# Optimization experiments

Hardware: AMD Instinct MI355X
Metric: run time of the kernel (lower is better)

Reference implementation:

```python
import jax, jax.numpy as jnp
import numpy as np
from jax import lax

B, S, D_IN, D_STATE, D_OUT, N_HEADS = 4, 2048, 2048, 2048, 2048, 16
H = D_STATE // N_HEADS  # 128


def setup_inputs() -> dict:
    key = jax.random.key(0)
    k1, k2, k3, k4, k5 = jax.random.split(key, 5)
    x = jax.random.normal(k1, (B, S, D_IN), dtype=jnp.float32)
    Wi = jax.random.normal(k2, (D_IN, D_STATE), dtype=jnp.float32) * (D_IN ** -0.5)
    b = jax.random.normal(k3, (D_STATE,), dtype=jnp.float32) * 0.01
    # state_weight is init'd with normal_ in torch; scale down for numerical sanity
    state_w = jax.random.normal(k4, (N_HEADS, H, H), dtype=jnp.float32) * (H ** -0.5)
    Wo = jax.random.normal(k5, (D_STATE, D_OUT), dtype=jnp.float32) * (D_STATE ** -0.5)
    input_state = jnp.zeros((B, D_STATE), dtype=jnp.float32)
    return {"x": x, "input_state": input_state, "Wi": Wi, "b": b,
            "state_w": state_w, "Wo": Wo}


def _rnn_forward(x, input_state, Wi, b, state_w, Wo):
    # input projection: [B,S,D_IN] -> [B,S,N,H]
    xp = (jnp.einsum('bsd,de->bse', x, Wi) + b).reshape(B, S, N_HEADS, H)
    h0 = input_state.reshape(B, N_HEADS, H)

    def step(h, xt):  # h: [B,N,H], xt: [B,N,H]
        h = jnp.tanh(jnp.einsum('bnh,nhk->bnk', h, state_w) + xt)
        return h, h

    _, hs = lax.scan(step, h0, jnp.moveaxis(xp, 1, 0))  # hs: [S,B,N,H]
    hs = jnp.moveaxis(hs, 0, 1)                         # [B,S,N,H]
    output_state = hs[:, -1].reshape(B, D_STATE)        # [B, state_size]
    out = jnp.einsum('bsd,de->bse', hs.reshape(B, S, D_STATE), Wo)
    return out, output_state


def reference(x, input_state, Wi, b, state_w, Wo):
    return _rnn_forward(x, input_state, Wi, b, state_w, Wo)
```

## Files before the change

kernel.cpp:

```cpp
#include <hip/hip_runtime.h>
#include <hip/hip_bf16.h>

#define B_ 4
#define S_ 2048
#define DIN 2048
#define DST 2048
#define DOUT 2048
#define NH 16
#define HH 128
#define M_ (B_ * S_)
#define OUT_OFF ((size_t)M_ * DOUT)

typedef __attribute__((ext_vector_type(8))) __bf16 bf16x8;
typedef __attribute__((ext_vector_type(4))) float f32x4;
typedef __attribute__((ext_vector_type(2))) _Float16 f16x2;

__device__ __forceinline__ unsigned short f2bf(float f) {
    unsigned int u = __float_as_uint(f);
    unsigned int r = u + 0x7FFFu + ((u >> 16) & 1u);
    return (unsigned short)(r >> 16);
}
__device__ __forceinline__ unsigned pk16(_Float16 a, _Float16 b) {
    return (unsigned)__builtin_bit_cast(unsigned short, a) |
           ((unsigned)__builtin_bit_cast(unsigned short, b) << 16);
}

__device__ __forceinline__ float fdot2(f16x2 a, f16x2 b, float c) {
#if __has_builtin(__builtin_amdgcn_fdot2)
    return __builtin_amdgcn_fdot2(a, b, c, false);
#else
    return fmaf((float)a.x, (float)b.x, fmaf((float)a.y, (float)b.y, c));
#endif
}
__device__ __forceinline__ float fdu(unsigned h, unsigned w, float c) {
    return fdot2(__builtin_bit_cast(f16x2, h), __builtin_bit_cast(f16x2, w), c);
}

__device__ __forceinline__ void gload_lds16(const void* g, void* l) {
    __builtin_amdgcn_global_load_lds(
        (const __attribute__((address_space(1))) void*)g,
        (__attribute__((address_space(3))) void*)l, 16, 0, 0);
}

__global__ __launch_bounds__(256) void k_transpose_bf16(
    const float* __restrict__ in, unsigned short* __restrict__ out, int K, int N) {
    __shared__ float tile[64][65];
    int k0 = blockIdx.y * 64, n0 = blockIdx.x * 64;
    int tr  = threadIdx.x >> 4;
    int tc4 = (threadIdx.x & 15) * 4;
#pragma unroll
    for (int p = 0; p < 4; ++p) {
        int r = tr + p * 16;
        float4 v = *(const float4*)&in[(size_t)(k0 + r) * N + n0 + tc4];
        tile[r][tc4 + 0] = v.x; tile[r][tc4 + 1] = v.y;
        tile[r][tc4 + 2] = v.z; tile[r][tc4 + 3] = v.w;
    }
    __syncthreads();
#pragma unroll
    for (int p = 0; p < 4; ++p) {
        int n = tr + p * 16;
        ushort4 o;
        o.x = f2bf(tile[tc4 + 0][n]); o.y = f2bf(tile[tc4 + 1][n]);
        o.z = f2bf(tile[tc4 + 2][n]); o.w = f2bf(tile[tc4 + 3][n]);
        *(ushort4*)&out[(size_t)(n0 + n) * K + k0 + tc4] = o;
    }
}

__global__ __launch_bounds__(256, 2) void k_gemm1(
    const float* __restrict__ x,
    const unsigned short* __restrict__ Bt,
    unsigned short* __restrict__ xpf,
    const float* __restrict__ bias) {
    __shared__ unsigned short As[128 * 64];
    __shared__ unsigned short Bs[128 * 64];
    const int tid  = threadIdx.x;
    const int lane = tid & 63;
    const int wid  = tid >> 6;
    const int wr = wid >> 1, wc = wid & 1;
    const int row0 = blockIdx.y * 128, col0 = blockIdx.x * 128;

    f32x4 acc[4][4];
#pragma unroll
    for (int m = 0; m < 4; ++m)
#pragma unroll
        for (int n = 0; n < 4; ++n) acc[m][n] = (f32x4)(0.f);

    const float* Ab = x + (size_t)row0 * DIN;
    const char* Bb = (const char*)(Bt + (size_t)col0 * DIN);

    int srow[4], skb[4];
#pragma unroll
    for (int i = 0; i < 4; ++i) {
        unsigned o = (unsigned)(i * 256 + tid) * 16u;
        unsigned l = o ^ (((o >> 7) & 7u) << 4);
        srow[i] = (int)(l >> 7);
        skb[i]  = (int)(l & 127u);
    }

    for (int kt = 0; kt < DIN; kt += 64) {
#pragma unroll
        for (int i = 0; i < 8; ++i) {
            int idx = i * 256 + tid;
            int row = idx >> 4;
            int cc  = (idx & 15) * 4;
            float4 v = *(const float4*)&Ab[(size_t)row * DIN + kt + cc];
            ushort4 u;
            u.x = f2bf(v.x); u.y = f2bf(v.y); u.z = f2bf(v.z); u.w = f2bf(v.w);
            unsigned byte = (unsigned)(row * 128 + cc * 2);
            byte ^= ((unsigned)(row & 7)) << 4;
            *(ushort4*)((char*)As + byte) = u;
        }
#pragma unroll
        for (int i = 0; i < 4; ++i) {
            unsigned o = (unsigned)(i * 256 + tid) * 16u;
            gload_lds16(Bb + (size_t)srow[i] * (DIN * 2) + (size_t)kt * 2 + skb[i],
                        (char*)Bs + o);
        }
        asm volatile("s_waitcnt vmcnt(0)" ::: "memory");
        __syncthreads();
#pragma unroll
        for (int ks = 0; ks < 2; ++ks) {
            bf16x8 af[4], bfr[4];
#pragma unroll
            for (int m = 0; m < 4; ++m) {
                int row = wr * 64 + m * 16 + (lane & 15);
                unsigned o = (unsigned)(row * 128 + ks * 64 + ((lane >> 4) * 16));
                o ^= ((unsigned)(row & 7) << 4);
                af[m] = *(const bf16x8*)((const char*)As + o);
            }
#pragma unroll
            for (int n = 0; n < 4; ++n) {
                int col = wc * 64 + n * 16 + (lane & 15);
                unsigned o = (unsigned)(col * 128 + ks * 64 + ((lane >> 4) * 16));
                o ^= ((unsigned)(col & 7) << 4);
                bfr[n] = *(const bf16x8*)((const char*)Bs + o);
            }
#pragma unroll
            for (int m = 0; m < 4; ++m)
#pragma unroll
                for (int n = 0; n < 4; ++n)
                    acc[m][n] = __builtin_amdgcn_mfma_f32_16x16x32_bf16(
                        af[m], bfr[n], acc[m][n], 0, 0, 0);
        }
        __syncthreads();
    }

#pragma unroll
    for (int n = 0; n < 4; ++n) {
        int gcol = col0 + wc * 64 + n * 16 + (lane & 15);
        float bv = bias[gcol];
#pragma unroll
        for (int m = 0; m < 4; ++m) {
            int growb = row0 + wr * 64 + m * 16 + ((lane >> 4) * 4);
#pragma unroll
            for (int r = 0; r < 4; ++r) {
                float v = acc[m][n][r] + bv;
                xpf[(size_t)(growb + r) * DST + gcol] =
                    __builtin_bit_cast(unsigned short, (_Float16)v);
            }
        }
    }
}

__global__ __launch_bounds__(256, 2) void k_gemm2(
    const unsigned short* __restrict__ A,
    const unsigned short* __restrict__ Bt,
    float* __restrict__ C) {
    __shared__ unsigned short As[128 * 64];
    __shared__ unsigned short Bs[128 * 64];
    const int tid  = threadIdx.x;
    const int lane = tid & 63;
    const int wid  = tid >> 6;
    const int wr = wid >> 1, wc = wid & 1;
    const int row0 = blockIdx.y * 128, col0 = blockIdx.x * 128;

    f32x4 acc[4][4];
#pragma unroll
    for (int m = 0; m < 4; ++m)
#pragma unroll
        for (int n = 0; n < 4; ++n) acc[m][n] = (f32x4)(0.f);

    const char* Abase = (const char*)(A + (size_t)row0 * DST);
    const char* Bbase = (const char*)(Bt + (size_t)col0 * DST);

    int srow[4], skb[4];
#pragma unroll
    for (int i = 0; i < 4; ++i) {
        unsigned o = (unsigned)(i * 256 + tid) * 16u;
        unsigned l = o ^ (((o >> 7) & 7u) << 4);
        srow[i] = (int)(l >> 7);
        skb[i]  = (int)(l & 127u);
    }

    for (int kt = 0; kt < DST; kt += 64) {
#pragma unroll
        for (int i = 0; i < 4; ++i) {
            unsigned o = (unsigned)(i * 256 + tid) * 16u;
            gload_lds16(Abase + (size_t)srow[i] * (DST * 2) + (size_t)kt * 2 + skb[i],
                        (char*)As + o);
            gload_lds16(Bbase + (size_t)srow[i] * (DST * 2) + (size_t)kt * 2 + skb[i],
                        (char*)Bs + o);
        }
        asm volatile("s_waitcnt vmcnt(0)" ::: "memory");
        __syncthreads();
#pragma unroll
        for (int ks = 0; ks < 2; ++ks) {
            bf16x8 af[4], bfr[4];
#pragma unroll
            for (int m = 0; m < 4; ++m) {
                int row = wr * 64 + m * 16 + (lane & 15);
                unsigned o = (unsigned)(row * 128 + ks * 64 + ((lane >> 4) * 16));
                o ^= ((unsigned)(row & 7) << 4);
                af[m] = *(const bf16x8*)((const char*)As + o);
            }
#pragma unroll
            for (int n = 0; n < 4; ++n) {
                int col = wc * 64 + n * 16 + (lane & 15);
                unsigned o = (unsigned)(col * 128 + ks * 64 + ((lane >> 4) * 16));
                o ^= ((unsigned)(col & 7) << 4);
                bfr[n] = *(const bf16x8*)((const char*)Bs + o);
            }
#pragma unroll
            for (int m = 0; m < 4; ++m)
#pragma unroll
                for (int n = 0; n < 4; ++n)
                    acc[m][n] = __builtin_amdgcn_mfma_f32_16x16x32_bf16(
                        af[m], bfr[n], acc[m][n], 0, 0, 0);
        }
        __syncthreads();
    }

#pragma unroll
    for (int n = 0; n < 4; ++n) {
        int gcol = col0 + wc * 64 + n * 16 + (lane & 15);
#pragma unroll
        for (int m = 0; m < 4; ++m) {
            int growb = row0 + wr * 64 + m * 16 + ((lane >> 4) * 4);
            float* cp = C + (size_t)growb * DOUT + gcol;
#pragma unroll
            for (int r = 0; r < 4; ++r) cp[(size_t)r * DOUT] = acc[m][n][r];
        }
    }
}

__global__ __attribute__((amdgpu_flat_work_group_size(64, 64),
                          amdgpu_waves_per_eu(1, 1))) void k_scan(
    const unsigned short* __restrict__ xpf,
    const float* __restrict__ h0,
    const float* __restrict__ sw,
    unsigned short* __restrict__ hsb,
    float* __restrict__ out_state) {
    __shared__ __align__(16) unsigned hb[64];
    const int l = threadIdx.x;
    const int bb = blockIdx.x >> 4;
    const int nn = blockIdx.x & 15;
    const int c0 = l * 2;

    const float* wb = sw + (size_t)nn * HH * HH;

    unsigned wu[128];
#pragma unroll
    for (int k = 0; k < 64; ++k) {
        float2 rA = *(const float2*)&wb[(size_t)(2 * k) * HH + c0];
        float2 rB = *(const float2*)&wb[(size_t)(2 * k + 1) * HH + c0];
        unsigned a = pk16((_Float16)rA.x, (_Float16)rB.x);
        unsigned b = pk16((_Float16)rA.y, (_Float16)rB.y);
        asm volatile("" : "+v"(a));
        asm volatile("" : "+v"(b));
        wu[k] = a;
        wu[64 + k] = b;
    }

    {
        float2 h2 = *(const float2*)&h0[bb * DST + nn * HH + c0];
        hb[l] = pk16((_Float16)h2.x, (_Float16)h2.y);
    }

    const unsigned* xrow = (const unsigned*)(xpf + (size_t)bb * S_ * DST + nn * HH) + l;
    unsigned* hrow = (unsigned*)(hsb + (size_t)bb * S_ * DST + nn * HH) + l;
    float* osp = out_state + bb * DST + nn * HH + c0;

    unsigned x0 = xrow[0], x1 = xrow[1024], x2 = xrow[2048], x3 = xrow[3072];

    const uint4* hp = (const uint4*)hb;

    for (int t = 0; t < S_; ++t) {
        int tpf = (t + 4 < S_) ? t + 4 : S_ - 1;
        unsigned x4 = xrow[(size_t)tpf * 1024];

        float a0 = 0.f, a1 = 0.f, a2 = 0.f, a3 = 0.f;
        float b0 = 0.f, b1 = 0.f, b2 = 0.f, b3 = 0.f;
#pragma unroll
        for (int j = 0; j < 16; ++j) {
            uint4 H = hp[j];
            a0 = fdu(H.x, wu[4 * j + 0], a0); b0 = fdu(H.x, wu[64 + 4 * j + 0], b0);
            a1 = fdu(H.y, wu[4 * j + 1], a1); b1 = fdu(H.y, wu[64 + 4 * j + 1], b1);
            a2 = fdu(H.z, wu[4 * j + 2], a2); b2 = fdu(H.z, wu[64 + 4 * j + 2], b2);
            a3 = fdu(H.w, wu[4 * j + 3], a3); b3 = fdu(H.w, wu[64 + 4 * j + 3], b3);
        }

        f16x2 xv = __builtin_bit_cast(f16x2, x0);
        float s0 = ((a0 + a1) + (a2 + a3)) + (float)xv.x;
        float s1 = ((b0 + b1) + (b2 + b3)) + (float)xv.y;
        float e0 = __builtin_amdgcn_exp2f(s0 * 2.885390081777927f);
        float e1 = __builtin_amdgcn_exp2f(s1 * 2.885390081777927f);
        float th0 = fmaf(-2.f, __builtin_amdgcn_rcpf(e0 + 1.f), 1.f);
        float th1 = fmaf(-2.f, __builtin_amdgcn_rcpf(e1 + 1.f), 1.f);

        hb[l] = pk16((_Float16)th0, (_Float16)th1);
        hrow[(size_t)t * (DST / 2)] = (unsigned)f2bf(th0) | ((unsigned)f2bf(th1) << 16);
        if (t == S_ - 1) { osp[0] = th0; osp[1] = th1; }

        x0 = x1; x1 = x2; x2 = x3; x3 = x4;
    }
}

extern "C" void kernel_launch(void* const* d_in, const int* in_sizes, int n_in,
                              void* d_out, int out_size, void* d_ws, size_t ws_size,
                              hipStream_t stream) {
    const float* x    = (const float*)d_in[0];
    const float* h0   = (const float*)d_in[1];
    const float* Wi   = (const float*)d_in[2];
    const float* bias = (const float*)d_in[3];
    const float* sw   = (const float*)d_in[4];
    const float* Wo   = (const float*)d_in[5];
    float* out = (float*)d_out;

    char* ws = (char*)d_ws;
    unsigned short* hsb = (unsigned short*)ws;
    unsigned short* wit = (unsigned short*)(ws + 33554432);
    unsigned short* wot = (unsigned short*)(ws + 41943040);
    unsigned short* xpf = (unsigned short*)(ws + 50331648);

    dim3 tg(32, 32);
    k_transpose_bf16<<<tg, 256, 0, stream>>>(Wi, wit, DIN, DST);
    k_transpose_bf16<<<tg, 256, 0, stream>>>(Wo, wot, DST, DOUT);
    dim3 g1(DST / 128, M_ / 128);
    k_gemm1<<<g1, 256, 0, stream>>>(x, wit, xpf, bias);
    k_scan<<<64, 64, 0, stream>>>(xpf, h0, sw, hsb, out + OUT_OFF);
    dim3 g2(DOUT / 128, M_ / 128);
    k_gemm2<<<g2, 256, 0, stream>>>(hsb, wot, out);
}
```

Baseline: 1.043 ms.

## Rewrite recurrent scan with MFMA per head, batching all batch rows

Replaces the per-(batch, head) single-wave scan, which used fdot2 with weights held in registers, with one 256-thread block per head. Each step computes the recurrent matvec for all 4 batch rows at once using 16x16x32 f16 MFMA, padding the batch dimension to 16. The hidden state is double-buffered in swizzled LDS with one barrier per step. This cuts the ALU dot-product work on the serial critical path, at the cost of a block barrier each step, 12 of 16 MFMA columns wasted on padding, and only 16 blocks running.

```diff
diff --git a/kernel.cpp b/kernel.cpp
--- a/kernel.cpp
+++ b/kernel.cpp
@@ -14,6 +14,7 @@
 typedef __attribute__((ext_vector_type(8))) __bf16 bf16x8;
 typedef __attribute__((ext_vector_type(4))) float f32x4;
 typedef __attribute__((ext_vector_type(2))) _Float16 f16x2;
+typedef __attribute__((ext_vector_type(8))) _Float16 f16x8;
 
 __device__ __forceinline__ unsigned short f2bf(float f) {
     unsigned int u = __float_as_uint(f);
@@ -23,17 +24,6 @@
 __device__ __forceinline__ unsigned pk16(_Float16 a, _Float16 b) {
     return (unsigned)__builtin_bit_cast(unsigned short, a) |
            ((unsigned)__builtin_bit_cast(unsigned short, b) << 16);
-}
-
-__device__ __forceinline__ float fdot2(f16x2 a, f16x2 b, float c) {
-#if __has_builtin(__builtin_amdgcn_fdot2)
-    return __builtin_amdgcn_fdot2(a, b, c, false);
-#else
-    return fmaf((float)a.x, (float)b.x, fmaf((float)a.y, (float)b.y, c));
-#endif
-}
-__device__ __forceinline__ float fdu(unsigned h, unsigned w, float c) {
-    return fdot2(__builtin_bit_cast(f16x2, h), __builtin_bit_cast(f16x2, w), c);
 }
 
 __device__ __forceinline__ void gload_lds16(const void* g, void* l) {
@@ -243,75 +233,131 @@
     }
 }
 
-__global__ __attribute__((amdgpu_flat_work_group_size(64, 64),
-                          amdgpu_waves_per_eu(1, 1))) void k_scan(
+__global__ __attribute__((amdgpu_flat_work_group_size(256, 256))) void k_scan_mfma(
     const unsigned short* __restrict__ xpf,
     const float* __restrict__ h0,
     const float* __restrict__ sw,
     unsigned short* __restrict__ hsb,
     float* __restrict__ out_state) {
-    __shared__ __align__(16) unsigned hb[64];
-    const int l = threadIdx.x;
-    const int bb = blockIdx.x >> 4;
-    const int nn = blockIdx.x & 15;
-    const int c0 = l * 2;
-
-    const float* wb = sw + (size_t)nn * HH * HH;
-
-    unsigned wu[128];
-#pragma unroll
-    for (int k = 0; k < 64; ++k) {
-        float2 rA = *(const float2*)&wb[(size_t)(2 * k) * HH + c0];
-        float2 rB = *(const float2*)&wb[(size_t)(2 * k + 1) * HH + c0];
-        unsigned a = pk16((_Float16)rA.x, (_Float16)rB.x);
-        unsigned b = pk16((_Float16)rA.y, (_Float16)rB.y);
-        asm volatile("" : "+v"(a));
-        asm volatile("" : "+v"(b));
-        wu[k] = a;
-        wu[64 + k] = b;
-    }
-
+    __shared__ __align__(16) char hbuf[2][4096];
+    const int tid  = threadIdx.x;
+    const int lane = tid & 63;
+    const int wid  = tid >> 6;
+    const int hh   = blockIdx.x;
+    const float* wb = sw + (size_t)hh * HH * HH;
+
+    f16x8 wf[2][4];
+#pragma unroll
+    for (int tau = 0; tau < 2; ++tau) {
+        int n = (2 * wid + tau) * 16 + (lane & 15);
+#pragma unroll
+        for (int ks = 0; ks < 4; ++ks) {
+            f16x8 v;
+#pragma unroll
+            for (int j = 0; j < 8; ++j) {
+                int k = ks * 32 + (lane >> 4) * 8 + j;
+                v[j] = (_Float16)wb[(size_t)k * HH + n];
+            }
+            wf[tau][ks] = v;
+        }
+    }
+
+#pragma unroll
+    for (int i = 0; i < 4; ++i) {
+        ((unsigned*)hbuf[0])[i * 256 + tid] = 0u;
+        ((unsigned*)hbuf[1])[i * 256 + tid] = 0u;
+    }
+    __syncthreads();
     {
-        float2 h2 = *(const float2*)&h0[bb * DST + nn * HH + c0];
-        hb[l] = pk16((_Float16)h2.x, (_Float16)h2.y);
-    }
-
-    const unsigned* xrow = (const unsigned*)(xpf + (size_t)bb * S_ * DST + nn * HH) + l;
-    unsigned* hrow = (unsigned*)(hsb + (size_t)bb * S_ * DST + nn * HH) + l;
-    float* osp = out_state + bb * DST + nn * HH + c0;
-
-    unsigned x0 = xrow[0], x1 = xrow[1024], x2 = xrow[2048], x3 = xrow[3072];
-
-    const uint4* hp = (const uint4*)hb;
-
+        int b = tid >> 6, k2 = tid & 63;
+        float2 v = *(const float2*)&h0[(size_t)b * DST + hh * HH + 2 * k2];
+        unsigned byte = (unsigned)(b * 256 + k2 * 4) ^ ((unsigned)(b & 7) << 4);
+        *(unsigned*)(hbuf[0] + byte) = pk16((_Float16)v.x, (_Float16)v.y);
+    }
+    __syncthreads();
+
+    const int bB = lane & 15;
+    const int ch = lane >> 4;
+    const bool act = (bB < 4);
+    const int nq0 = (2 * wid + 0) * 16 + ch * 4;
+    const int nq1 = (2 * wid + 1) * 16 + ch * 4;
+
+    const unsigned short* xA = xpf + (size_t)bB * S_ * DST + hh * HH + nq0;
+    const unsigned short* xB = xpf + (size_t)bB * S_ * DST + hh * HH + nq1;
+    unsigned short* hA = hsb + (size_t)bB * S_ * DST + hh * HH + nq0;
+    unsigned short* hB = hsb + (size_t)bB * S_ * DST + hh * HH + nq1;
+
+    uint2 xA0, xA1, xB0, xB1;
+    if (act) {
+        xA0 = *(const uint2*)(xA);                 xB0 = *(const uint2*)(xB);
+        xA1 = *(const uint2*)(xA + (size_t)DST);   xB1 = *(const uint2*)(xB + (size_t)DST);
+    }
+
+    int p = 0;
     for (int t = 0; t < S_; ++t) {
-        int tpf = (t + 4 < S_) ? t + 4 : S_ - 1;
-        unsigned x4 = xrow[(size_t)tpf * 1024];
-
-        float a0 = 0.f, a1 = 0.f, a2 = 0.f, a3 = 0.f;
-        float b0 = 0.f, b1 = 0.f, b2 = 0.f, b3 = 0.f;
-#pragma unroll
-        for (int j = 0; j < 16; ++j) {
-            uint4 H = hp[j];
-            a0 = fdu(H.x, wu[4 * j + 0], a0); b0 = fdu(H.x, wu[64 + 4 * j + 0], b0);
-            a1 = fdu(H.y, wu[4 * j + 1], a1); b1 = fdu(H.y, wu[64 + 4 * j + 1], b1);
-            a2 = fdu(H.z, wu[4 * j + 2], a2); b2 = fdu(H.z, wu[64 + 4 * j + 2], b2);
-            a3 = fdu(H.w, wu[4 * j + 3], a3); b3 = fdu(H.w, wu[64 + 4 * j + 3], b3);
-        }
-
-        f16x2 xv = __builtin_bit_cast(f16x2, x0);
-        float s0 = ((a0 + a1) + (a2 + a3)) + (float)xv.x;
-        float s1 = ((b0 + b1) + (b2 + b3)) + (float)xv.y;
-        float e0 = __builtin_amdgcn_exp2f(s0 * 2.885390081777927f);
-        float e1 = __builtin_amdgcn_exp2f(s1 * 2.885390081777927f);
-        float th0 = fmaf(-2.f, __builtin_amdgcn_rcpf(e0 + 1.f), 1.f);
-        float th1 = fmaf(-2.f, __builtin_amdgcn_rcpf(e1 + 1.f), 1.f);
-
-        hb[l] = pk16((_Float16)th0, (_Float16)th1);
-        hrow[(size_t)t * (DST / 2)] = (unsigned)f2bf(th0) | ((unsigned)f2bf(th1) << 16);
-        if (t == S_ - 1) { osp[0] = th0; osp[1] = th1; }
-
-        x0 = x1; x1 = x2; x2 = x3; x3 = x4;
+        f16x8 hf0, hf1, hf2, hf3;
+        {
+            unsigned base = (unsigned)(bB * 256 + ch * 16) ^ ((unsigned)(bB & 7) << 4);
+            hf0 = __builtin_bit_cast(f16x8, *(const uint4*)(hbuf[p] + (base ^ 0)));
+            hf1 = __builtin_bit_cast(f16x8, *(const uint4*)(hbuf[p] + (base ^ 64)));
+            hf2 = __builtin_bit_cast(f16x8, *(const uint4*)(hbuf[p] + (base ^ 128)));
+            hf3 = __builtin_bit_cast(f16x8, *(const uint4*)(hbuf[p] + (base ^ 192)));
+        }
+        f32x4 acc0 = (f32x4)(0.f), acc1 = (f32x4)(0.f);
+        acc0 = __builtin_amdgcn_mfma_f32_16x16x32_f16(wf[0][0], hf0, acc0, 0, 0, 0);
+        acc1 = __builtin_amdgcn_mfma_f32_16x16x32_f16(wf[1][0], hf0, acc1, 0, 0, 0);
+        acc0 = __builtin_amdgcn_mfma_f32_16x16x32_f16(wf[0][1], hf1, acc0, 0, 0, 0);
+        acc1 = __builtin_amdgcn_mfma_f32_16x16x32_f16(wf[1][1], hf1, acc1, 0, 0, 0);
+        acc0 = __builtin_amdgcn_mfma_f32_16x16x32_f16(wf[0][2], hf2, acc0, 0, 0, 0);
+        acc1 = __builtin_amdgcn_mfma_f32_16x16x32_f16(wf[1][2], hf2, acc1, 0, 0, 0);
+        acc0 = __builtin_amdgcn_mfma_f32_16x16x32_f16(wf[0][3], hf3, acc0, 0, 0, 0);
+        acc1 = __builtin_amdgcn_mfma_f32_16x16x32_f16(wf[1][3], hf3, acc1, 0, 0, 0);
+
+        if (act) {
+            int tp = (t + 2 < S_) ? t + 2 : S_ - 1;
+            uint2 xA2 = *(const uint2*)(xA + (size_t)tp * DST);
+            uint2 xB2 = *(const uint2*)(xB + (size_t)tp * DST);
+
+            f16x2 a_lo = __builtin_bit_cast(f16x2, xA0.x);
+            f16x2 a_hi = __builtin_bit_cast(f16x2, xA0.y);
+            f16x2 b_lo = __builtin_bit_cast(f16x2, xB0.x);
+            f16x2 b_hi = __builtin_bit_cast(f16x2, xB0.y);
+            float s0 = acc0[0] + (float)a_lo.x, s1 = acc0[1] + (float)a_lo.y;
+            float s2 = acc0[2] + (float)a_hi.x, s3 = acc0[3] + (float)a_hi.y;
+            float s4 = acc1[0] + (float)b_lo.x, s5 = acc1[1] + (float)b_lo.y;
+            float s6 = acc1[2] + (float)b_hi.x, s7 = acc1[3] + (float)b_hi.y;
+
+#define TANH(s) fmaf(-2.f, __builtin_amdgcn_rcpf( \
+            __builtin_amdgcn_exp2f((s) * 2.885390081777927f) + 1.f), 1.f)
+            float t0 = TANH(s0), t1 = TANH(s1), t2 = TANH(s2), t3 = TANH(s3);
+            float t4 = TANH(s4), t5 = TANH(s5), t6 = TANH(s6), t7 = TANH(s7);
+#undef TANH
+
+            unsigned byte0 = (unsigned)(bB * 256 + nq0 * 2) ^ ((unsigned)(bB & 7) << 4);
+            unsigned byte1 = (unsigned)(bB * 256 + nq1 * 2) ^ ((unsigned)(bB & 7) << 4);
+            uint2 w0 = {pk16((_Float16)t0, (_Float16)t1), pk16((_Float16)t2, (_Float16)t3)};
+            uint2 w1 = {pk16((_Float16)t4, (_Float16)t5), pk16((_Float16)t6, (_Float16)t7)};
+            *(uint2*)(hbuf[p ^ 1] + byte0) = w0;
+            *(uint2*)(hbuf[p ^ 1] + byte1) = w1;
+
+            uint2 g0 = {(unsigned)f2bf(t0) | ((unsigned)f2bf(t1) << 16),
+                        (unsigned)f2bf(t2) | ((unsigned)f2bf(t3) << 16)};
+            uint2 g1 = {(unsigned)f2bf(t4) | ((unsigned)f2bf(t5) << 16),
+                        (unsigned)f2bf(t6) | ((unsigned)f2bf(t7) << 16)};
+            *(uint2*)(hA + (size_t)t * DST) = g0;
+            *(uint2*)(hB + (size_t)t * DST) = g1;
+
+            if (t == S_ - 1) {
+                float* o0 = out_state + (size_t)bB * DST + hh * HH + nq0;
+                float* o1 = out_state + (size_t)bB * DST + hh * HH + nq1;
+                *(float4*)o0 = float4{t0, t1, t2, t3};
+                *(float4*)o1 = float4{t4, t5, t6, t7};
+            }
+            xA0 = xA1; xA1 = xA2;
+            xB0 = xB1; xB1 = xB2;
+        }
+        asm volatile("s_waitcnt lgkmcnt(0)\ns_barrier" ::: "memory");
+        p ^= 1;
     }
 }
 
@@ -337,7 +383,7 @@
     k_transpose_bf16<<<tg, 256, 0, stream>>>(Wo, wot, DST, DOUT);
     dim3 g1(DST / 128, M_ / 128);
     k_gemm1<<<g1, 256, 0, stream>>>(x, wit, xpf, bias);
-    k_scan<<<64, 64, 0, stream>>>(xpf, h0, sw, hsb, out + OUT_OFF);
+    k_scan_mfma<<<NH, 256, 0, stream>>>(xpf, h0, sw, hsb, out + OUT_OFF);
     dim3 g2(DOUT / 128, M_ / 128);
     k_gemm2<<<g2, 256, 0, stream>>>(hsb, wot, out);
 }
```

Measured after the change: 1.149 ms. 1.1x slower.
